# Kernel tuning notes

Measured on AMD Instinct MI355X. Metric: run time of the kernel, lower is better.

## Reference

```python
import jax, jax.numpy as jnp
import numpy as np

D = 512

def _resmlp(x, W1, W2):
    # residual MLP: x + silu(x W1) W2  (e3nn-style bias-free linears)
    return x + jax.nn.silu(x @ W1) @ W2

def setup_inputs() -> dict:
    key = jax.random.key(0)
    ks = jax.random.split(key, 12)
    s = 1.0 / np.sqrt(D)
    mk = lambda k: jax.random.normal(k, (D, D), dtype=jnp.float32) * s
    return {
        "x": jax.random.normal(ks[0], (4, 4096, D), dtype=jnp.float32),
        "qW1": mk(ks[1]), "qW2": mk(ks[2]),
        "kW1": mk(ks[3]), "kW2": mk(ks[4]),
        "vW1": mk(ks[5]), "vW2": mk(ks[6]),
        "aWq": mk(ks[7]), "aWk": mk(ks[8]), "aWv": mk(ks[9]),
        "Wout": mk(ks[10]),
    }

def reference(x, qW1, qW2, kW1, kW2, vW1, vW2, aWq, aWk, aWv, Wout):
    # ResiMLP q/k/v projections on node features [B, N, D]
    q = _resmlp(x, qW1, qW2) @ aWq
    k = _resmlp(x, kW1, kW2) @ aWk
    v = _resmlp(x, vW1, vW2) @ aWv
    # naive full attention: bmm -> softmax(dim=1, over QUERY axis) -> bmm
    attn = jnp.einsum("bqd,bkd->bqk", q, k)   # [B, Nq, Nk]
    attn = jax.nn.softmax(attn, axis=1)        # faithful to Softmax(dim=1)
    out = jnp.einsum("bqk,bkd->bqd", attn, v)  # [B, N, D]
    return out @ Wout
```

## Files before the change

### kernel.cpp

```cpp
#include <hip/hip_runtime.h>
#include <hip/hip_bf16.h>
#include <stdint.h>
#include <stddef.h>

typedef _Float16 f16;
typedef __attribute__((ext_vector_type(8))) _Float16 f16x8;
typedef __attribute__((ext_vector_type(4))) float f32x4;

#define EPI_NONE 0
#define EPI_SILU 1
#define EPI_RES  2
#define OUT_F16    0
#define OUT_F32    1
#define OUT_VT     3
#define OUT_ESTATS 4

__device__ __forceinline__ void gll16(const f16* g, char* l) {
    __builtin_amdgcn_global_load_lds(
        (const __attribute__((address_space(1))) void*)g,
        (__attribute__((address_space(3))) void*)l, 16, 0, 0);
}

template<int BN, int EPI, int OUT, int AEC>
__global__ __launch_bounds__(256)
void gemm_f16(const f16* __restrict__ A, const f16* __restrict__ Bm,
              void* __restrict__ Cp, const float* __restrict__ Res,
              float* __restrict__ mp, float* __restrict__ zp,
              const float* __restrict__ cScale,
              int kseg, int lda, int ldb, int ldc, int ldr,
              unsigned long long sA, unsigned long long sB, unsigned long long sC)
{
    constexpr int NWF = BN / 32;

    const f16* Ag = A + (size_t)blockIdx.z * sA;
    const f16* Bg = Bm + (size_t)blockIdx.z * sB;
    const size_t zC = (size_t)blockIdx.z * sC;

    unsigned nwg = gridDim.x * gridDim.y;
    unsigned lin = blockIdx.y * gridDim.x + blockIdx.x;
    unsigned cpx = nwg >> 3;
    unsigned swz = (lin & 7) * cpx + (lin >> 3);
    unsigned bxs = swz % gridDim.x, bys = swz / gridDim.x;

    const int t    = threadIdx.x;
    const int w    = t >> 6;
    const int lane = t & 63;
    const int wr   = w >> 1, wc = w & 1;
    const int lo   = lane & 15, hi = lane >> 4;
    const int brow = bys * 128;
    const int bcol = bxs * BN;

    __shared__ f16 As[128 * 64];
    __shared__ f16 Bs[BN * 64];
    __shared__ float smst[(OUT == OUT_ESTATS) ? 512 : 4];

    f32x4 acc[4][NWF];
#pragma unroll
    for (int m = 0; m < 4; ++m)
#pragma unroll
        for (int n = 0; n < NWF; ++n)
            acc[m][n] = (f32x4){0.f, 0.f, 0.f, 0.f};

    const int r0 = t >> 3;
    const int cswz = ((t & 7) ^ ((t >> 3) & 7)) * 8;
    const int rA7  = lo & 7;

    const float* cb = nullptr;
    f16x8 bq[NWF];
    float4 cq0, cq1;
    if constexpr (AEC) {
        cb = cScale + ((size_t)blockIdx.z * 32 + (brow >> 7)) * 4096;
#pragma unroll
        for (int i = 0; i < NWF; ++i)
            bq[i] = *(const f16x8*)(Bg + (size_t)(bcol + i * 32 + r0) * ldb + cswz);
        cq0 = *(const float4*)(cb + cswz);
        cq1 = *(const float4*)(cb + cswz + 4);
    }

    for (int k0 = 0; k0 < kseg; k0 += 64) {
#pragma unroll
        for (int i = 0; i < 4; ++i)
            gll16(Ag + (size_t)(brow + i * 32 + r0) * lda + (k0 + cswz),
                  (char*)As + i * 4096 + w * 1024);
        if constexpr (AEC) {
            float cf[8] = {cq0.x, cq0.y, cq0.z, cq0.w, cq1.x, cq1.y, cq1.z, cq1.w};
#pragma unroll
            for (int i = 0; i < NWF; ++i) {
                f16x8 ev = bq[i], pv;
#pragma unroll
                for (int j = 0; j < 8; ++j) pv[j] = (f16)((float)ev[j] * cf[j]);
                *(f16x8*)((char*)Bs + i * 4096 + t * 16) = pv;
            }
            if (k0 + 64 < kseg) {
#pragma unroll
                for (int i = 0; i < NWF; ++i)
                    bq[i] = *(const f16x8*)(Bg + (size_t)(bcol + i * 32 + r0) * ldb
                                            + (k0 + 64 + cswz));
                cq0 = *(const float4*)(cb + k0 + 64 + cswz);
                cq1 = *(const float4*)(cb + k0 + 64 + cswz + 4);
            }
        } else {
#pragma unroll
            for (int i = 0; i < NWF; ++i)
                gll16(Bg + (size_t)(bcol + i * 32 + r0) * ldb + (k0 + cswz),
                      (char*)Bs + i * 4096 + w * 1024);
        }
        __syncthreads();

#pragma unroll
        for (int kk = 0; kk < 64; kk += 32) {
            f16x8 aH[4], bH[NWF];
#pragma unroll
            for (int m = 0; m < 4; ++m) {
                int idx = (wr * 64 + m * 16 + lo) * 64 +
                          ((((kk >> 3) + hi) ^ rA7) * 8);
                aH[m] = *(const f16x8*)&As[idx];
            }
#pragma unroll
            for (int n = 0; n < NWF; ++n) {
                int idx = (wc * (BN / 2) + n * 16 + lo) * 64 +
                          ((((kk >> 3) + hi) ^ rA7) * 8);
                bH[n] = *(const f16x8*)&Bs[idx];
            }
#pragma unroll
            for (int m = 0; m < 4; ++m)
#pragma unroll
                for (int n = 0; n < NWF; ++n)
                    acc[m][n] = __builtin_amdgcn_mfma_f32_16x16x32_f16(
                        aH[m], bH[n], acc[m][n], 0, 0, 0);
        }
        __syncthreads();
    }

    if constexpr (OUT == OUT_ESTATS) {
        float mb[NWF];
#pragma unroll
        for (int n = 0; n < NWF; ++n) {
            float ml = acc[0][n][0];
#pragma unroll
            for (int m = 0; m < 4; ++m)
#pragma unroll
                for (int j = 0; j < 4; ++j) ml = fmaxf(ml, acc[m][n][j]);
            ml = fmaxf(ml, __shfl_xor(ml, 16));
            ml = fmaxf(ml, __shfl_xor(ml, 32));
            if (hi == 0) smst[wr * 128 + wc * (BN / 2) + n * 16 + lo] = ml;
        }
        __syncthreads();
#pragma unroll
        for (int n = 0; n < NWF; ++n) {
            int c = wc * (BN / 2) + n * 16 + lo;
            mb[n] = fmaxf(smst[c], smst[128 + c]);
        }
        float zsum[NWF];
#pragma unroll
        for (int n = 0; n < NWF; ++n) {
            zsum[n] = 0.f;
            int col = bcol + wc * (BN / 2) + n * 16 + lo;
#pragma unroll
            for (int m = 0; m < 4; ++m)
#pragma unroll
                for (int j = 0; j < 4; ++j) {
                    int row = brow + wr * 64 + m * 16 + hi * 4 + j;
                    float e = __expf(acc[m][n][j] - mb[n]);
                    zsum[n] += e;
                    ((f16*)Cp)[(size_t)row * ldc + col] = (f16)e;
                }
        }
        __syncthreads();
#pragma unroll
        for (int n = 0; n < NWF; ++n) {
            float zl = zsum[n];
            zl += __shfl_xor(zl, 16);
            zl += __shfl_xor(zl, 32);
            if (hi == 0) smst[256 + wr * 128 + wc * (BN / 2) + n * 16 + lo] = zl;
        }
        __syncthreads();
        if (t < 128) {
            float m0 = smst[t],       m1 = smst[128 + t];
            float z0 = smst[256 + t], z1 = smst[384 + t];
            size_t o = (size_t)(brow >> 7) * 4096 + bcol + t;
            mp[o] = fmaxf(m0, m1);
            zp[o] = z0 + z1;
        }
        return;
    }

#pragma unroll
    for (int m = 0; m < 4; ++m) {
#pragma unroll
        for (int n = 0; n < NWF; ++n) {
            if constexpr (OUT == OUT_VT) {
                int row0 = brow + wr * 64 + m * 16 + hi * 4;
                int col  = bcol + wc * (BN / 2) + n * 16 + lo;
                int bb = row0 >> 12, n0 = row0 & 4095;
                unsigned short u[4];
#pragma unroll
                for (int j = 0; j < 4; ++j) {
                    f16 vb = (f16)acc[m][n][j];
                    u[j] = *(unsigned short*)&vb;
                }
                ushort4 pack = {u[0], u[1], u[2], u[3]};
                *(ushort4*)&((f16*)Cp)[((size_t)(bb * 512 + col) << 12) + n0] = pack;
            } else {
#pragma unroll
                for (int j = 0; j < 4; ++j) {
                    int row = brow + wr * 64 + m * 16 + hi * 4 + j;
                    int col = bcol + wc * (BN / 2) + n * 16 + lo;
                    size_t idx = (size_t)row * ldc + col + zC;
                    float v = acc[m][n][j];
                    if (EPI == EPI_SILU) v = v / (1.f + __expf(-v));
                    if (EPI == EPI_RES)  v += Res[(size_t)row * ldr + col];
                    if (OUT == OUT_F32) ((float*)Cp)[idx] = v;
                    else                ((f16*)Cp)[idx] = (f16)v;
                }
            }
        }
    }
}

__global__ void cast_x_kernel(const float* __restrict__ x, f16* __restrict__ xf)
{
    size_t i = ((size_t)blockIdx.x * 256 + threadIdx.x) * 8;
    float4 a = *(const float4*)(x + i);
    float4 b = *(const float4*)(x + i + 4);
    f16x8 o;
    o[0] = (f16)a.x; o[1] = (f16)a.y; o[2] = (f16)a.z; o[3] = (f16)a.w;
    o[4] = (f16)b.x; o[5] = (f16)b.y; o[6] = (f16)b.z; o[7] = (f16)b.w;
    *(f16x8*)(xf + i) = o;
}

struct WPack { const float* W[10]; f16* H[10]; };

__global__ void transw_all_kernel(WPack p)
{
    const float* W = p.W[blockIdx.z];
    f16* WT = p.H[blockIdx.z];
    __shared__ float tile[32][33];
    int bx = blockIdx.x * 32, by = blockIdx.y * 32;
    int tx = threadIdx.x, ty = threadIdx.y;
#pragma unroll
    for (int i = 0; i < 32; i += 8)
        tile[ty + i][tx] = W[(size_t)(by + ty + i) * 512 + bx + tx];
    __syncthreads();
#pragma unroll
    for (int i = 0; i < 32; i += 8)
        WT[(size_t)(bx + ty + i) * 512 + by + tx] = (f16)tile[tx][ty + i];
}

__global__ void colstats_comb_kernel(const float* __restrict__ mp,
                                     const float* __restrict__ zp,
                                     float* __restrict__ cB)
{
    int col = blockIdx.x * 256 + threadIdx.x;
    float m = -1e30f;
#pragma unroll
    for (int i = 0; i < 32; ++i) m = fmaxf(m, mp[i * 4096 + col]);
    float z = 0.f;
#pragma unroll
    for (int i = 0; i < 32; ++i) z += zp[i * 4096 + col] * __expf(mp[i * 4096 + col] - m);
    float r = 1.f / z;
#pragma unroll
    for (int i = 0; i < 32; ++i)
        cB[i * 4096 + col] = __expf(mp[i * 4096 + col] - m) * r;
}

extern "C" void kernel_launch(void* const* d_in, const int* in_sizes, int n_in,
                              void* d_out, int out_size, void* d_ws, size_t ws_size,
                              hipStream_t stream)
{
    const int B = 4, N = 4096, D = 512;
    const size_t MALL = (size_t)B * N;
    const size_t ND = MALL * D;
    const size_t NN = (size_t)N * N;
    const size_t WW = (size_t)D * D;
    const float* x = (const float*)d_in[0];
    const float* Wf[10];
    for (int i = 0; i < 10; ++i) Wf[i] = (const float*)d_in[1 + i];

    char* ws = (char*)d_ws;
    size_t off = 0;
    auto carve = [&](size_t bytes) -> char* {
        char* p = ws + off;
        off = (off + bytes + 255) & ~(size_t)255;
        return p;
    };

    const size_t PLANE = NN * 2;
    f16* A0 = (f16*)carve(PLANE);
    f16* A1 = (f16*)carve(PLANE);
    f16* A2 = (f16*)carve(PLANE);
    f16* A3 = (f16*)carve(PLANE);
    f16* F  = (f16*)carve(PLANE);
    f16* G  = (f16*)carve(PLANE);
    f16* wc1 = (f16*)carve(2 * WW * 2);
    f16* wc2 = (f16*)carve(2 * WW * 2);
    f16* wcA = (f16*)carve(2 * WW * 2);
    f16* wv1 = (f16*)carve(WW * 2);
    f16* wv2 = (f16*)carve(WW * 2);
    f16* wv3 = (f16*)carve(WW * 2);
    f16* wo  = (f16*)carve(WW * 2);
    float* mp = (float*)carve(32 * 4096 * 4);
    float* zp = (float*)carve(32 * 4096 * 4);
    float* cB = (float*)carve((size_t)B * 32 * 4096 * 4);

    f16* xf  = A0;
    f16* t1v = A1;  f16* hv = A1 + ND;
    f16* t1  = A2;
    f16* h   = A3;
    f16* QKf = F;
    f16* VT  = G;   f16* O = G + (size_t)B * D * N;
    f16* E_all = A0;
    (void)in_sizes; (void)n_in; (void)out_size; (void)ws_size;

    cast_x_kernel<<<dim3((unsigned)(ND / 2048)), 256, 0, stream>>>(x, xf);
    WPack wp;
    wp.W[0] = Wf[0]; wp.H[0] = wc1;
    wp.W[1] = Wf[2]; wp.H[1] = wc1 + WW;
    wp.W[2] = Wf[1]; wp.H[2] = wc2;
    wp.W[3] = Wf[3]; wp.H[3] = wc2 + WW;
    wp.W[4] = Wf[6]; wp.H[4] = wcA;
    wp.W[5] = Wf[7]; wp.H[5] = wcA + WW;
    wp.W[6] = Wf[4]; wp.H[6] = wv1;
    wp.W[7] = Wf[5]; wp.H[7] = wv2;
    wp.W[8] = Wf[8]; wp.H[8] = wv3;
    wp.W[9] = Wf[9]; wp.H[9] = wo;
    transw_all_kernel<<<dim3(16, 16, 10), dim3(32, 8), 0, stream>>>(wp);

    gemm_f16<64, EPI_SILU, OUT_F16, 0><<<dim3(8, 128), 256, 0, stream>>>(
        xf, wv1, t1v, nullptr, nullptr, nullptr, nullptr,
        512, 512, 512, 512, 512, 0, 0, 0);
    gemm_f16<64, EPI_RES, OUT_F16, 0><<<dim3(8, 128), 256, 0, stream>>>(
        t1v, wv2, hv, x, nullptr, nullptr, nullptr,
        512, 512, 512, 512, 512, 0, 0, 0);
    gemm_f16<64, EPI_NONE, OUT_VT, 0><<<dim3(8, 128), 256, 0, stream>>>(
        hv, wv3, VT, nullptr, nullptr, nullptr, nullptr,
        512, 512, 512, 512, 512, 0, 0, 0);

    gemm_f16<64, EPI_SILU, OUT_F16, 0><<<dim3(16, 128), 256, 0, stream>>>(
        xf, wc1, t1, nullptr, nullptr, nullptr, nullptr,
        512, 512, 512, 1024, 512, 0, 0, 0);
    gemm_f16<64, EPI_RES, OUT_F16, 0><<<dim3(8, 128, 2), 256, 0, stream>>>(
        t1, wc2, h, x, nullptr, nullptr, nullptr,
        512, 1024, 512, 1024, 512, 512, WW, 512);
    gemm_f16<64, EPI_NONE, OUT_F16, 0><<<dim3(8, 128, 2), 256, 0, stream>>>(
        h, wcA, QKf, nullptr, nullptr, nullptr, nullptr,
        512, 1024, 512, 1024, 512, 512, WW, 512);

    for (int b = 0; b < B; ++b) {
        size_t boff = (size_t)b * N * 1024;
        gemm_f16<128, EPI_NONE, OUT_ESTATS, 0><<<dim3(32, 32), 256, 0, stream>>>(
            QKf + boff, QKf + boff + 512,
            E_all + (size_t)b * NN, nullptr, mp, zp, nullptr,
            512, 1024, 1024, 4096, 4096, 0, 0, 0);
        colstats_comb_kernel<<<16, 256, 0, stream>>>(
            mp, zp, cB + (size_t)b * 32 * 4096);
    }

    gemm_f16<64, EPI_NONE, OUT_F16, 1><<<dim3(8, 32, 4), 256, 0, stream>>>(
        E_all, VT, O, nullptr, nullptr, nullptr, cB,
        4096, 4096, 4096, 512, 512,
        NN, (unsigned long long)D * N, (unsigned long long)N * D);

    gemm_f16<64, EPI_NONE, OUT_F32, 0><<<dim3(8, 128), 256, 0, stream>>>(
        O, wo, d_out, nullptr, nullptr, nullptr, nullptr,
        512, 512, 512, 512, 512, 0, 0, 0);
}
```

Before: 425.8 us.

## Merge q/k/v projection GEMMs, batch score kernel over z, widen tiles

```diff
diff --git a/kernel.cpp b/kernel.cpp
--- a/kernel.cpp
+++ b/kernel.cpp
@@ -133,6 +133,7 @@
     }
 
     if constexpr (OUT == OUT_ESTATS) {
+        const size_t zS = (size_t)blockIdx.z * (32 * 4096);
         float mb[NWF];
 #pragma unroll
         for (int n = 0; n < NWF; ++n) {
@@ -163,7 +164,7 @@
                     int row = brow + wr * 64 + m * 16 + hi * 4 + j;
                     float e = __expf(acc[m][n][j] - mb[n]);
                     zsum[n] += e;
-                    ((f16*)Cp)[(size_t)row * ldc + col] = (f16)e;
+                    ((f16*)Cp)[(size_t)row * ldc + col + zC] = (f16)e;
                 }
         }
         __syncthreads();
@@ -178,7 +179,7 @@
         if (t < 128) {
             float m0 = smst[t],       m1 = smst[128 + t];
             float z0 = smst[256 + t], z1 = smst[384 + t];
-            size_t o = (size_t)(brow >> 7) * 4096 + bcol + t;
+            size_t o = zS + (size_t)(brow >> 7) * 4096 + bcol + t;
             mp[o] = fmaxf(m0, m1);
             zp[o] = z0 + z1;
         }
@@ -251,17 +252,19 @@
                                      const float* __restrict__ zp,
                                      float* __restrict__ cB)
 {
+    size_t base = (size_t)blockIdx.y * (32 * 4096);
     int col = blockIdx.x * 256 + threadIdx.x;
     float m = -1e30f;
 #pragma unroll
-    for (int i = 0; i < 32; ++i) m = fmaxf(m, mp[i * 4096 + col]);
+    for (int i = 0; i < 32; ++i) m = fmaxf(m, mp[base + i * 4096 + col]);
     float z = 0.f;
 #pragma unroll
-    for (int i = 0; i < 32; ++i) z += zp[i * 4096 + col] * __expf(mp[i * 4096 + col] - m);
+    for (int i = 0; i < 32; ++i)
+        z += zp[base + i * 4096 + col] * __expf(mp[base + i * 4096 + col] - m);
     float r = 1.f / z;
 #pragma unroll
     for (int i = 0; i < 32; ++i)
-        cB[i * 4096 + col] = __expf(mp[i * 4096 + col] - m) * r;
+        cB[base + i * 4096 + col] = __expf(mp[base + i * 4096 + col] - m) * r;
 }
 
 extern "C" void kernel_launch(void* const* d_in, const int* in_sizes, int n_in,
@@ -286,82 +289,63 @@
     };
 
     const size_t PLANE = NN * 2;
-    f16* A0 = (f16*)carve(PLANE);
-    f16* A1 = (f16*)carve(PLANE);
-    f16* A2 = (f16*)carve(PLANE);
-    f16* A3 = (f16*)carve(PLANE);
-    f16* F  = (f16*)carve(PLANE);
-    f16* G  = (f16*)carve(PLANE);
-    f16* wc1 = (f16*)carve(2 * WW * 2);
-    f16* wc2 = (f16*)carve(2 * WW * 2);
-    f16* wcA = (f16*)carve(2 * WW * 2);
-    f16* wv1 = (f16*)carve(WW * 2);
-    f16* wv2 = (f16*)carve(WW * 2);
-    f16* wv3 = (f16*)carve(WW * 2);
-    f16* wo  = (f16*)carve(WW * 2);
-    float* mp = (float*)carve(32 * 4096 * 4);
-    float* zp = (float*)carve(32 * 4096 * 4);
-    float* cB = (float*)carve((size_t)B * 32 * 4096 * 4);
-
-    f16* xf  = A0;
-    f16* t1v = A1;  f16* hv = A1 + ND;
-    f16* t1  = A2;
-    f16* h   = A3;
-    f16* QKf = F;
-    f16* VT  = G;   f16* O = G + (size_t)B * D * N;
-    f16* E_all = A0;
+    f16* E_all = (f16*)carve(4 * PLANE);
+    f16* QKf   = (f16*)carve(PLANE);
+    f16* VT    = (f16*)carve((size_t)B * D * N * 2);
+    f16* O     = (f16*)carve(ND * 2);
+    f16* wc1   = (f16*)carve(3 * WW * 2);
+    f16* wc2   = (f16*)carve(3 * WW * 2);
+    f16* wcA   = (f16*)carve(2 * WW * 2);
+    f16* wv3   = (f16*)carve(WW * 2);
+    f16* wo    = (f16*)carve(WW * 2);
+    float* mp  = (float*)carve((size_t)B * 32 * 4096 * 4);
+    float* zp  = (float*)carve((size_t)B * 32 * 4096 * 4);
+    float* cB  = (float*)carve((size_t)B * 32 * 4096 * 4);
+
+    f16* xf = E_all;
+    f16* t1 = E_all + ND;
+    f16* h  = t1 + MALL * 1536;
     (void)in_sizes; (void)n_in; (void)out_size; (void)ws_size;
 
     cast_x_kernel<<<dim3((unsigned)(ND / 2048)), 256, 0, stream>>>(x, xf);
     WPack wp;
     wp.W[0] = Wf[0]; wp.H[0] = wc1;
     wp.W[1] = Wf[2]; wp.H[1] = wc1 + WW;
-    wp.W[2] = Wf[1]; wp.H[2] = wc2;
-    wp.W[3] = Wf[3]; wp.H[3] = wc2 + WW;
-    wp.W[4] = Wf[6]; wp.H[4] = wcA;
-    wp.W[5] = Wf[7]; wp.H[5] = wcA + WW;
-    wp.W[6] = Wf[4]; wp.H[6] = wv1;
-    wp.W[7] = Wf[5]; wp.H[7] = wv2;
+    wp.W[2] = Wf[4]; wp.H[2] = wc1 + 2 * WW;
+    wp.W[3] = Wf[1]; wp.H[3] = wc2;
+    wp.W[4] = Wf[3]; wp.H[4] = wc2 + WW;
+    wp.W[5] = Wf[5]; wp.H[5] = wc2 + 2 * WW;
+    wp.W[6] = Wf[6]; wp.H[6] = wcA;
+    wp.W[7] = Wf[7]; wp.H[7] = wcA + WW;
     wp.W[8] = Wf[8]; wp.H[8] = wv3;
     wp.W[9] = Wf[9]; wp.H[9] = wo;
     transw_all_kernel<<<dim3(16, 16, 10), dim3(32, 8), 0, stream>>>(wp);
 
-    gemm_f16<64, EPI_SILU, OUT_F16, 0><<<dim3(8, 128), 256, 0, stream>>>(
-        xf, wv1, t1v, nullptr, nullptr, nullptr, nullptr,
-        512, 512, 512, 512, 512, 0, 0, 0);
-    gemm_f16<64, EPI_RES, OUT_F16, 0><<<dim3(8, 128), 256, 0, stream>>>(
-        t1v, wv2, hv, x, nullptr, nullptr, nullptr,
-        512, 512, 512, 512, 512, 0, 0, 0);
-    gemm_f16<64, EPI_NONE, OUT_VT, 0><<<dim3(8, 128), 256, 0, stream>>>(
-        hv, wv3, VT, nullptr, nullptr, nullptr, nullptr,
-        512, 512, 512, 512, 512, 0, 0, 0);
-
-    gemm_f16<64, EPI_SILU, OUT_F16, 0><<<dim3(16, 128), 256, 0, stream>>>(
+    gemm_f16<128, EPI_SILU, OUT_F16, 0><<<dim3(12, 128), 256, 0, stream>>>(
         xf, wc1, t1, nullptr, nullptr, nullptr, nullptr,
-        512, 512, 512, 1024, 512, 0, 0, 0);
-    gemm_f16<64, EPI_RES, OUT_F16, 0><<<dim3(8, 128, 2), 256, 0, stream>>>(
+        512, 512, 512, 1536, 512, 0, 0, 0);
+    gemm_f16<128, EPI_RES, OUT_F16, 0><<<dim3(4, 128, 3), 256, 0, stream>>>(
         t1, wc2, h, x, nullptr, nullptr, nullptr,
-        512, 1024, 512, 1024, 512, 512, WW, 512);
-    gemm_f16<64, EPI_NONE, OUT_F16, 0><<<dim3(8, 128, 2), 256, 0, stream>>>(
+        512, 1536, 512, 1536, 512, 512, WW, 512);
+    gemm_f16<128, EPI_NONE, OUT_F16, 0><<<dim3(4, 128, 2), 256, 0, stream>>>(
         h, wcA, QKf, nullptr, nullptr, nullptr, nullptr,
-        512, 1024, 512, 1024, 512, 512, WW, 512);
-
-    for (int b = 0; b < B; ++b) {
-        size_t boff = (size_t)b * N * 1024;
-        gemm_f16<128, EPI_NONE, OUT_ESTATS, 0><<<dim3(32, 32), 256, 0, stream>>>(
-            QKf + boff, QKf + boff + 512,
-            E_all + (size_t)b * NN, nullptr, mp, zp, nullptr,
-            512, 1024, 1024, 4096, 4096, 0, 0, 0);
-        colstats_comb_kernel<<<16, 256, 0, stream>>>(
-            mp, zp, cB + (size_t)b * 32 * 4096);
-    }
+        512, 1536, 512, 1024, 512, 512, WW, 512);
+    gemm_f16<128, EPI_NONE, OUT_VT, 0><<<dim3(4, 128), 256, 0, stream>>>(
+        h + 1024, wv3, VT, nullptr, nullptr, nullptr, nullptr,
+        512, 1536, 512, 512, 512, 0, 0, 0);
+
+    gemm_f16<128, EPI_NONE, OUT_ESTATS, 0><<<dim3(32, 32, 4), 256, 0, stream>>>(
+        QKf, QKf + 512, E_all, nullptr, mp, zp, nullptr,
+        512, 1024, 1024, 4096, 4096,
+        (unsigned long long)N * 1024, (unsigned long long)N * 1024, NN);
+    colstats_comb_kernel<<<dim3(16, 4), 256, 0, stream>>>(mp, zp, cB);
 
     gemm_f16<64, EPI_NONE, OUT_F16, 1><<<dim3(8, 32, 4), 256, 0, stream>>>(
         E_all, VT, O, nullptr, nullptr, nullptr, cB,
         4096, 4096, 4096, 512, 512,
         NN, (unsigned long long)D * N, (unsigned long long)N * D);
 
-    gemm_f16<64, EPI_NONE, OUT_F32, 0><<<dim3(8, 128), 256, 0, stream>>>(
+    gemm_f16<128, EPI_NONE, OUT_F32, 0><<<dim3(4, 128), 256, 0, stream>>>(
         O, wo, d_out, nullptr, nullptr, nullptr, nullptr,
         512, 512, 512, 512, 512, 0, 0, 0);
 }
```

After: 377.3 us. 11.4% less time.
